# Kernel optimization log

Measured on AMD Instinct MI355X. Metric: run time of the kernel, lower is better.

The kernel has to match this reference:

```python
import jax, jax.numpy as jnp
import numpy as np

T, N = 128, 256
D_T, D_A, D_V = 768, 128, 512
H_T, H_A, H_V = 256, 128, 128
HD = H_T + H_A + H_V      # 512, concat hidden dim
MEM = 256
OUT = 1


def _lstm(x, h, c, Wih, Whh, bih, bhh):
    # torch.nn.LSTMCell: gates = x@Wih^T + bih + h@Whh^T + bhh, chunks (i,f,g,o)
    g = x @ Wih.T + bih + h @ Whh.T + bhh
    i, f, gg, o = jnp.split(g, 4, axis=1)
    c2 = jax.nn.sigmoid(f) * c + jax.nn.sigmoid(i) * jnp.tanh(gg)
    return jax.nn.sigmoid(o) * jnp.tanh(c2), c2


def _mlp(x, w1, b1, w2, b2):
    # Linear -> ReLU -> (dropout: identity in eval) -> Linear
    return jax.nn.relu(x @ w1.T + b1) @ w2.T + b2


def setup_inputs() -> dict:
    key = jax.random.key(0)
    ks = iter(jax.random.split(key, 48))
    def P(shape):
        return jax.random.normal(next(ks), shape, jnp.float32) * 0.05
    inp = {}
    inp["x_text"] = jax.random.normal(next(ks), (T, N, D_T), jnp.float32)
    inp["x_audio"] = jax.random.normal(next(ks), (T, N, D_A), jnp.float32)
    inp["x_vision"] = jax.random.normal(next(ks), (T, N, D_V), jnp.float32)
    inp["lengths"] = jax.random.randint(next(ks), (N,), 1, T + 1, jnp.int32)
    for nm, d, h in (("t", D_T, H_T), ("a", D_A, H_A), ("v", D_V, H_V)):
        inp[f"Wih_{nm}"] = P((4 * h, d))
        inp[f"Whh_{nm}"] = P((4 * h, h))
        inp[f"bih_{nm}"] = P((4 * h,))
        inp[f"bhh_{nm}"] = P((4 * h,))
    # attention MLP: 2*HD -> HD -> 2*HD
    inp["aw1"], inp["ab1"] = P((HD, 2 * HD)), P((HD,))
    inp["aw2"], inp["ab2"] = P((2 * HD, HD)), P((2 * HD,))
    # gamma1 / gamma2 / update MLPs: 2*HD -> HD -> MEM
    for pre in ("g1", "g2", "u"):
        inp[f"{pre}w1"], inp[f"{pre}b1"] = P((HD, 2 * HD)), P((HD,))
        inp[f"{pre}w2"], inp[f"{pre}b2"] = P((MEM, HD)), P((MEM,))
    # output MLP: (HD+MEM) -> (HD+MEM) -> OUT
    inp["ow1"], inp["ob1"] = P((HD + MEM, HD + MEM)), P((HD + MEM,))
    inp["ow2"], inp["ob2"] = P((OUT, HD + MEM)), P((OUT,))
    return inp


def reference(x_text, x_audio, x_vision, lengths,
              Wih_t, Whh_t, bih_t, bhh_t,
              Wih_a, Whh_a, bih_a, bhh_a,
              Wih_v, Whh_v, bih_v, bhh_v,
              aw1, ab1, aw2, ab2,
              g1w1, g1b1, g1w2, g1b2,
              g2w1, g2b1, g2w2, g2b2,
              uw1, ub1, uw2, ub2,
              ow1, ob1, ow2, ob2):
    n = x_text.shape[1]

    def step(carry, xs):
        ht, ct, ha, ca, hv, cv, mem = carry
        xt, xa, xv = xs
        prev_cc = jnp.concatenate([ct, ca, cv], axis=1)           # [N, HD]
        ht, ct = _lstm(xt, ht, ct, Wih_t, Whh_t, bih_t, bhh_t)
        ha, ca = _lstm(xa, ha, ca, Wih_a, Whh_a, bih_a, bhh_a)
        hv, cv = _lstm(xv, hv, cv, Wih_v, Whh_v, bih_v, bhh_v)
        cc = jnp.concatenate([ct, ca, cv], axis=1)                # [N, HD]
        cc_tt = jnp.concatenate([prev_cc, cc], axis=1)            # [N, 2*HD]
        attn = jax.nn.softmax(_mlp(cc_tt, aw1, ab1, aw2, ab2), axis=1)
        cc_star = cc_tt * attn
        g1 = jax.nn.sigmoid(_mlp(cc_star, g1w1, g1b1, g1w2, g1b2))
        g2 = jax.nn.sigmoid(_mlp(cc_star, g2w1, g2b1, g2w2, g2b2))
        u = jnp.tanh(_mlp(cc_star, uw1, ub1, uw2, ub2))
        mem = g1 * mem + g2 * u
        return (ht, ct, ha, ca, hv, cv, mem), (ht, ha, hv, mem)

    z = lambda h: jnp.zeros((n, h), x_text.dtype)
    carry0 = (z(H_T), z(H_T), z(H_A), z(H_A), z(H_V), z(H_V), z(MEM))
    _, (Ht, Ha, Hv, Ms) = jax.lax.scan(step, carry0, (x_text, x_audio, x_vision))

    idx = lengths - 1                 # per-sample last valid step
    rows = jnp.arange(n)
    hT = jnp.concatenate([Ht[idx, rows], Ha[idx, rows], Hv[idx, rows]], axis=1)
    o = jnp.concatenate([hT, Ms[idx, rows]], axis=1)   # [N, HD+MEM]
    return _mlp(o, ow1, ob1, ow2, ob2)
```

## Files before the change

kernel.cpp:

```cpp
#include <hip/hip_runtime.h>
#include <math.h>

#define TT 128
#define NN 256

typedef __attribute__((ext_vector_type(8))) short short8;
typedef __attribute__((ext_vector_type(8))) _Float16 half8;
typedef __attribute__((ext_vector_type(4))) float f32x4;

#define LOG2E 1.44269504088896340736f

__device__ __forceinline__ float exp2_(float x){ return __builtin_amdgcn_exp2f(x); }
__device__ __forceinline__ float rcp_(float x){ return __builtin_amdgcn_rcpf(x); }
__device__ __forceinline__ float sig_(float x){
  return rcp_(1.f + exp2_(-LOG2E*x));
}
__device__ __forceinline__ float tanh_(float x){
  const float e = exp2_(2.f*LOG2E*fabsf(x));
  const float t = 1.f - 2.f*rcp_(e + 1.f);
  return copysignf(t, x);
}
__device__ __forceinline__ float bf2f(unsigned int u){ return __uint_as_float(u<<16); }
__device__ __forceinline__ unsigned short f2bf(float x){
  unsigned int u = __float_as_uint(x);
  u += 0x7fffu + ((u>>16)&1u);
  return (unsigned short)(u>>16);
}
__device__ __forceinline__ unsigned short f2h(float x){
  _Float16 h = (_Float16)x;
  return __builtin_bit_cast(unsigned short, h);
}
__device__ __forceinline__ float h2f(unsigned short u){
  _Float16 h = __builtin_bit_cast(_Float16, u);
  return (float)h;
}
__device__ __forceinline__ unsigned int cvtpk_f16(float a, float b){
  unsigned int r;
  asm("v_cvt_pkrtz_f16_f32 %0, %1, %2" : "=v"(r) : "v"(a), "v"(b));
  return r;
}

__device__ __forceinline__ void gld_lds16(const unsigned short* g, unsigned short* l){
  __builtin_amdgcn_global_load_lds(
      (const __attribute__((address_space(1))) unsigned int*)(g),
      (__attribute__((address_space(3))) unsigned int*)(l), 16, 0, 0);
}

__device__ __forceinline__ short8 ld_llc8s(const unsigned short* p){
  f32x4 r;
  asm volatile("global_load_dwordx4 %0, %1, off sc0 sc1" : "=v"(r) : "v"(p) : "memory");
  return __builtin_bit_cast(short8, r);
}
__device__ __forceinline__ void st_llc_s(unsigned short* p, unsigned short v){
  unsigned int vv = v;
  asm volatile("global_store_short %0, %1, off sc0 sc1" :: "v"(p), "v"(vv) : "memory");
}

template<int BM,int BN,int ACT>
__global__ __launch_bounds__(256) void gemm_nt(const float* __restrict__ A,
    const float* __restrict__ W, const float* __restrict__ b1,
    const float* __restrict__ b2, float* __restrict__ C,
    int M, int K, int Nc)
{
  constexpr int TM = BM/16, TN = BN/16;
  __shared__ float As[BM*32];
  __shared__ float Bs[BN*32];
  const int tid = threadIdx.x;
  const int n0 = blockIdx.x*BN, m0 = blockIdx.y*BM;
  const int tx = tid & 15, ty = tid >> 4;
  float acc[TM][TN];
  #pragma unroll
  for (int r=0;r<TM;r++)
    #pragma unroll
    for (int c=0;c<TN;c++) acc[r][c]=0.f;
  const int swA = (ty & 7) << 2;
  const int swB = (tx & 7) << 2;
  for (int k0=0;k0<K;k0+=32){
    #pragma unroll
    for (int f=tid; f<BM*8; f+=256){
      const int row=f>>3, kq=f&7;
      float4 v = *(const float4*)(A + (size_t)(m0+row)*K + k0 + (kq<<2));
      *(float4*)(&As[row*32 + ((kq<<2) ^ ((row&7)<<2))]) = v;
    }
    #pragma unroll
    for (int f=tid; f<BN*8; f+=256){
      const int row=f>>3, kq=f&7;
      float4 v = *(const float4*)(W + (size_t)(n0+row)*K + k0 + (kq<<2));
      *(float4*)(&Bs[row*32 + ((kq<<2) ^ ((row&7)<<2))]) = v;
    }
    __syncthreads();
    #pragma unroll
    for (int kq=0;kq<8;kq++){
      const int k = kq<<2;
      float4 av[TM], bv[TN];
      #pragma unroll
      for (int r=0;r<TM;r++){ const int row=ty+16*r; av[r] = *(const float4*)(&As[row*32 + (k ^ swA)]); }
      #pragma unroll
      for (int c=0;c<TN;c++){ const int col=tx+16*c; bv[c] = *(const float4*)(&Bs[col*32 + (k ^ swB)]); }
      #pragma unroll
      for (int r=0;r<TM;r++)
        #pragma unroll
        for (int c=0;c<TN;c++){
          acc[r][c] += av[r].x*bv[c].x;
          acc[r][c] += av[r].y*bv[c].y;
          acc[r][c] += av[r].z*bv[c].z;
          acc[r][c] += av[r].w*bv[c].w;
        }
    }
    __syncthreads();
  }
  #pragma unroll
  for (int c=0;c<TN;c++){
    const int gcol = n0 + tx + 16*c;
    const float bias = (b1 ? b1[gcol] : 0.f) + (b2 ? b2[gcol] : 0.f);
    #pragma unroll
    for (int r=0;r<TM;r++){
      const int grow = m0 + ty + 16*r;
      float v = acc[r][c] + bias;
      if (ACT==1) v = fmaxf(v, 0.f);
      C[(size_t)grow*Nc + gcol] = v;
    }
  }
}

template<int ACT,int OBF>
__global__ __launch_bounds__(256) void gemm_mfma(const unsigned short* __restrict__ A,
    const unsigned short* __restrict__ Wb, const float* __restrict__ bias,
    void* __restrict__ Cp, int M, int K, int Nc, int lda, int ldc, int aseg,
    int kswitch, int aextra)
{
  __shared__ unsigned short sA[128*64];
  __shared__ unsigned short sB[128*64];
  const int tid = threadIdx.x;
  const int wave = tid >> 6, lane = tid & 63;
  const int nx = gridDim.x;
  const int lin = blockIdx.y*nx + blockIdx.x;
  const int xcd = lin & 7, s = lin >> 3;
  const int ppx = gridDim.y >> 3;
  const int m0 = (xcd*ppx + s/nx)*128;
  const int n0 = (s % nx)*128;
  const unsigned short* Ab = A + (size_t)(n0 >> 8) * (size_t)aseg;
  const int wm = (wave>>1)*64, wn = (wave&1)*64;
  const int r = lane & 15, g = lane >> 4;
  const int srow = wave*32 + (lane>>3);
  const int scol = (((lane&7) ^ ((lane>>3)&7)) << 3);
  f32x4 acc[4][4];
  #pragma unroll
  for (int i=0;i<4;i++)
    #pragma unroll
    for (int j=0;j<4;j++) acc[i][j] = (f32x4){0.f,0.f,0.f,0.f};

  for (int k0 = 0; k0 < K; k0 += 64){
    const size_t aoff = (size_t)k0 + ((k0 >= kswitch) ? (size_t)aextra : 0);
    #pragma unroll
    for (int i=0;i<4;i++){
      gld_lds16(Ab + (size_t)(m0+srow+i*8)*lda + aoff + scol, &sA[wave*2048 + i*512]);
      gld_lds16(Wb + (size_t)(n0+srow+i*8)*K   + k0   + scol, &sB[wave*2048 + i*512]);
    }
    asm volatile("s_waitcnt vmcnt(0)" ::: "memory");
    __syncthreads();
    #pragma unroll
    for (int ks=0; ks<2; ks++){
      const int cofs = ((ks*32 + g*8) ^ ((r&7)<<3));
      short8 af[4], bfr[4];
      #pragma unroll
      for (int mi=0;mi<4;mi++) af[mi]  = *(const short8*)(&sA[(wm+mi*16+r)*64 + cofs]);
      #pragma unroll
      for (int ni=0;ni<4;ni++) bfr[ni] = *(const short8*)(&sB[(wn+ni*16+r)*64 + cofs]);
      #pragma unroll
      for (int mi=0;mi<4;mi++)
        #pragma unroll
        for (int ni=0;ni<4;ni++)
          acc[mi][ni] = __builtin_amdgcn_mfma_f32_16x16x32_bf16(af[mi], bfr[ni], acc[mi][ni], 0, 0, 0);
    }
    __syncthreads();
  }
  #pragma unroll
  for (int mi=0;mi<4;mi++)
    #pragma unroll
    for (int ni=0;ni<4;ni++){
      const int col_l = wn + ni*16 + r;
      const float b = bias[n0 + col_l];
      #pragma unroll
      for (int reg=0;reg<4;reg++){
        const int row = m0 + wm + mi*16 + g*4 + reg;
        float v = acc[mi][ni][reg] + b;
        if (ACT==1) v = fmaxf(v,0.f);
        else if (ACT==2) v = sig_(v);
        else if (ACT==3) v = tanh_(v);
        else if (ACT==4) v = (n0 + col_l < 512) ? sig_(v) : tanh_(v);
        if (OBF==1)      ((unsigned short*)Cp)[(size_t)row*ldc + n0 + col_l] = f2bf(v);
        else if (OBF==2) ((unsigned short*)Cp)[(size_t)row*ldc + n0 + col_l] = f2h(v);
        else             ((float*)Cp)[(size_t)row*ldc + n0 + col_l] = v;
      }
    }
}

__global__ __launch_bounds__(256) void proj_all(
    const float* __restrict__ xt, const float* __restrict__ xa, const float* __restrict__ xv,
    const unsigned short* __restrict__ wt, const unsigned short* __restrict__ wa,
    const unsigned short* __restrict__ wv,
    const float* __restrict__ bih_t, const float* __restrict__ bhh_t,
    const float* __restrict__ bih_a, const float* __restrict__ bhh_a,
    const float* __restrict__ bih_v, const float* __restrict__ bhh_v,
    unsigned short* __restrict__ Pt, unsigned short* __restrict__ Pa,
    unsigned short* __restrict__ Pv,
    const float* __restrict__ aw1, const float* __restrict__ aw2,
    const float* __restrict__ g1w1, const float* __restrict__ g2w1,
    const float* __restrict__ uw1, const float* __restrict__ g1w2,
    const float* __restrict__ g2w2, const float* __restrict__ uw2,
    unsigned short* __restrict__ wbp)
{
  __shared__ unsigned short sA[128*72];
  __shared__ unsigned short sB[128*64];
  const int tid = threadIdx.x;
  const int blk = blockIdx.x;
  if (blk >= 4096){
    const int cb = blk - 4096;
    const float* src; unsigned short* dst; int i;
    if (cb < 2560){
      const int s = cb >> 9, lb = cb & 511;
      src = (s==0)?aw1:(s==1)?aw2:(s==2)?g1w1:(s==3)?g2w1:uw1;
      dst = wbp + (size_t)s*524288;
      i = lb*256 + tid;
    } else {
      const int s = (cb-2560) >> 7, lb = (cb-2560) & 127;
      src = (s==0)?g1w2:(s==1)?g2w2:uw2;
      dst = wbp + 2621440 + (size_t)s*131072;
      i = lb*256 + tid;
    }
    const float4 v = ((const float4*)src)[i];
    ushort4 o;
    o.x=f2bf(v.x); o.y=f2bf(v.y); o.z=f2bf(v.z); o.w=f2bf(v.w);
    ((ushort4*)dst)[i] = o;
    return;
  }
  const int wave = tid >> 6, lane = tid & 63;
  const float* A; const unsigned short* Wf; const float *b1, *b2; unsigned short* C;
  int K, Nc, nbs, rel, shf;
  if (blk < 2048)      { rel=blk;      A=xt; Wf=wt; b1=bih_t; b2=bhh_t; C=Pt; K=768; Nc=1024; nbs=3; shf=8; }
  else if (blk < 3072) { rel=blk-2048; A=xa; Wf=wa; b1=bih_a; b2=bhh_a; C=Pa; K=128; Nc=512;  nbs=2; shf=7; }
  else                 { rel=blk-3072; A=xv; Wf=wv; b1=bih_v; b2=bhh_v; C=Pv; K=512; Nc=512;  nbs=2; shf=7; }
  const int xcd = rel & 7, s = rel >> 3;
  const int nxc = 1 << nbs;
  const int m0 = (xcd*32 + s/nxc)*128;
  const int n0 = (s & (nxc-1))*128;
  const int wm = (wave>>1)*64, wn = (wave&1)*64;
  const int r = lane & 15, g = lane >> 4;
  const int srow = wave*32 + (lane>>3);
  const int scol = (((lane&7) ^ ((lane>>3)&7)) << 3);
  f32x4 acc[4][4];
  #pragma unroll
  for (int i=0;i<4;i++)
    #pragma unroll
    for (int j=0;j<4;j++) acc[i][j] = (f32x4){0.f,0.f,0.f,0.f};

  for (int k0 = 0; k0 < K; k0 += 64){
    #pragma unroll
    for (int i=0;i<4;i++)
      gld_lds16(Wf + (size_t)(n0+srow+i*8)*K + k0 + scol, &sB[wave*2048 + i*512]);
    #pragma unroll
    for (int j=0;j<4;j++){
      const int slot = tid + j*256;
      const int row = slot>>3, seg = (slot&7)<<3;
      const float* ap = A + (size_t)(m0+row)*K + k0 + seg;
      const float4 v0 = *(const float4*)ap;
      const float4 v1 = *(const float4*)(ap+4);
      uint4 hv;
      hv.x = cvtpk_f16(v0.x, v0.y);
      hv.y = cvtpk_f16(v0.z, v0.w);
      hv.z = cvtpk_f16(v1.x, v1.y);
      hv.w = cvtpk_f16(v1.z, v1.w);
      *(uint4*)(&sA[row*72 + seg]) = hv;
    }
    asm volatile("s_waitcnt vmcnt(0)" ::: "memory");
    __syncthreads();
    #pragma unroll
    for (int ks=0; ks<2; ks++){
      const int cofsB = ((ks*32 + g*8) ^ ((r&7)<<3));
      half8 af[4], bfr[4];
      #pragma unroll
      for (int mi=0;mi<4;mi++) af[mi]  = *(const half8*)(&sA[(wm+mi*16+r)*72 + ks*32 + g*8]);
      #pragma unroll
      for (int ni=0;ni<4;ni++) bfr[ni] = *(const half8*)(&sB[(wn+ni*16+r)*64 + cofsB]);
      #pragma unroll
      for (int mi=0;mi<4;mi++)
        #pragma unroll
        for (int ni=0;ni<4;ni++)
          acc[mi][ni] = __builtin_amdgcn_mfma_f32_16x16x32_f16(af[mi], bfr[ni], acc[mi][ni], 0, 0, 0);
    }
    __syncthreads();
  }
  const int jm = (1<<shf) - 1;
  #pragma unroll
  for (int mi=0;mi<4;mi++)
    #pragma unroll
    for (int ni=0;ni<4;ni++){
      const int col_l = wn + ni*16 + r;
      const int col = n0 + col_l;
      const float b = b1[col] + b2[col];
      const size_t cofs = (size_t)((col & jm)<<2) + (col>>shf);
      #pragma unroll
      for (int reg=0;reg<4;reg++){
        const int row = m0 + wm + mi*16 + g*4 + reg;
        C[(size_t)row*Nc + cofs] = f2h(acc[mi][ni][reg] + b);
      }
    }
}

__device__ __forceinline__ void wfrag_body(const float* __restrict__ W, int H,
    int e, unsigned short* __restrict__ ff)
{
  const int nch = H >> 5;
  const int lane = e & 63;
  int r = e >> 6;
  const int ks = r % nch; r /= nch;
  const int ct = r & 3; r >>= 2;
  const int jb = r;
  const int col = ct*H + jb*16 + (lane & 15);
  const int kb  = ks*32 + (lane >> 4)*8;
  #pragma unroll
  for (int j=0;j<8;j++){
    ff[(size_t)e*8 + j] = f2h(W[(size_t)col*H + kb + j]);
  }
}

__global__ __launch_bounds__(256) void prep_all(
    const float* __restrict__ Wih_t, const float* __restrict__ Wih_a,
    const float* __restrict__ Wih_v,
    const float* __restrict__ Whh_t, const float* __restrict__ Whh_a,
    const float* __restrict__ Whh_v,
    const float* __restrict__ g1b1, const float* __restrict__ g2b1,
    const float* __restrict__ ub1,
    const float* __restrict__ g1b2, const float* __restrict__ g2b2,
    const float* __restrict__ ub2,
    unsigned short* __restrict__ wbp, unsigned short* __restrict__ wfp,
    float* __restrict__ bcat1, float* __restrict__ bcat2,
    float* __restrict__ hfZ,
    unsigned int* __restrict__ flags, unsigned short* __restrict__ ccb)
{
  const int blk = blockIdx.x, tid = threadIdx.x;
  if (blk < 1088){
    const int rel = blk;
    const float* src; unsigned short* dst; int i;
    if (rel < 768)      { src=Wih_t; dst=wbp+3014656; i=rel*256+tid; }
    else if (rel < 832) { src=Wih_a; dst=wbp+3801088; i=(rel-768)*256+tid; }
    else                { src=Wih_v; dst=wbp+3866624; i=(rel-832)*256+tid; }
    const float4 v = ((const float4*)src)[i];
    ushort4 h;
    h.x=f2h(v.x); h.y=f2h(v.y); h.z=f2h(v.z); h.w=f2h(v.w);
    ((ushort4*)dst)[i] = h;
  } else if (blk < 1280){
    const int rel = blk - 1088;
    if (rel < 128)      wfrag_body(Whh_t, 256, rel*256+tid,       wfp);
    else if (rel < 160) wfrag_body(Whh_a, 128, (rel-128)*256+tid, wfp+262144);
    else                wfrag_body(Whh_v, 128, (rel-160)*256+tid, wfp+327680);
  } else {
    const int rel = blk - 1280;
    if (rel < 6){
      const int idx = rel*256 + tid;
      float v = (idx<512) ? g1b1[idx] : (idx<1024) ? g2b1[idx-512] : ub1[idx-1024];
      bcat1[idx] = v;
    } else if (rel < 9){
      const int idx = (rel-6)*256 + tid;
      float v = (idx<256) ? g1b2[idx] : (idx<512) ? g2b2[idx-256] : ub2[idx-512];
      bcat2[idx] = v;
    } else if (rel < 265){
      const int i = (rel-9)*256 + tid;
      ((float4*)hfZ)[i] = (float4){0.f,0.f,0.f,0.f};
    } else if (rel < 271){
      const int i = (rel-265)*256 + tid;
      ((uint4*)flags)[i] = (uint4){0u,0u,0u,0u};
    } else {
      const int i = (rel-271)*256 + tid;
      ((uint4*)ccb)[i] = (uint4){0u,0u,0u,0u};
    }
  }
}

__global__ __launch_bounds__(256) void lstm_scan(
    const unsigned short* __restrict__ Pt, const unsigned short* __restrict__ Pa,
    const unsigned short* __restrict__ Pv,
    const unsigned short* __restrict__ wtfF, const unsigned short* __restrict__ wafF,
    const unsigned short* __restrict__ wvfF,
    const int* __restrict__ lengths,
    unsigned short* __restrict__ hfT, unsigned short* __restrict__ hfA, unsigned short* __restrict__ hfV,
    unsigned short* __restrict__ ccb, float* __restrict__ o_stage,
    unsigned int* __restrict__ flags)
{
  __shared__ unsigned short sWh[16384];
  __shared__ float sG[4*32*17];
  const int tid = threadIdx.x;
  const int b = blockIdx.x;
  const int rb = b & 7, jb = b >> 3;
  const int n0 = rb * 32;
  const unsigned short* P; const unsigned short* wfF; unsigned short* hf;
  int H, j0, off, grp, mem, gsz, jbl;
  if (jb < 16)      { P=Pt; wfF=wtfF; hf=hfT; H=256; jbl=jb;    off=0;   grp=rb;    mem=jbl; gsz=16; }
  else if (jb < 24) { P=Pa; wfF=wafF; hf=hfA; H=128; jbl=jb-16; off=256; grp=8+rb;  mem=jbl; gsz=8;  }
  else              { P=Pv; wfF=wvfF; hf=hfV; H=128; jbl=jb-24; off=384; grp=16+rb; mem=jbl; gsz=8;  }
  j0 = jbl*16;
  const int nch = H >> 5;
  const int G4 = 4*H;
  const size_t planeSz = (size_t)NN*H;
  unsigned int* myflag = &flags[(grp*16+mem)<<4];
  unsigned int* gflags = &flags[(grp*16)<<4];

  {
    const unsigned short* srcF = wfF + (size_t)jbl*4*nch*512;
    const int nseg = 4*nch*64;
    for (int s = tid; s < nseg; s += 256)
      *(uint4*)(&sWh[s*8]) = *(const uint4*)(srcF + (size_t)s*8);
  }
  const int tx = tid & 15, ty = tid >> 4;
  const int n_a = n0 + ty, n_b = n0 + ty + 16;
  const int last_a = lengths[n_a] - 1, last_b = lengths[n_b] - 1;
  const int jcol = j0 + tx;
  const int ksP = jcol >> 5, kqP = (jcol>>3)&3, jP = jcol&7;
  const size_t eA = ((size_t)((rb*2+0)*nch + ksP)*64 + (ty|(kqP<<4)))*8 + jP;
  const size_t eB = ((size_t)((rb*2+1)*nch + ksP)*64 + (ty|(kqP<<4)))*8 + jP;
  const int wave = tid >> 6, lane = tid & 63;
  const int rt = wave >> 1, ct0 = (wave&1)*2, ct1 = ct0+1;
  const size_t fragBase = ((size_t)(rb*2+rt)*nch)*512 + (size_t)lane*8;
  float c_a = 0.f, c_b = 0.f;
  uint2 pA, pB;
  {
    pA = *(const uint2*)(P + (size_t)n_a*G4 + (size_t)jcol*4);
    pB = *(const uint2*)(P + (size_t)n_b*G4 + (size_t)jcol*4);
  }
  __syncthreads();

  for (int t = 0; t < TT; ++t){
    const int cur = t & 1, nxt = cur ^ 1;
    const unsigned short* hH = hf + (size_t)cur*planeSz;
    short8 ah[8];
    #pragma unroll
    for (int ks=0; ks<8; ks++) if (ks < nch)
      ah[ks] = ld_llc8s(hH + fragBase + (size_t)ks*512);
    asm volatile("s_waitcnt vmcnt(0)" ::: "memory");
    uint2 pA2, pB2;
    if (t < TT-1){
      pA2 = *(const uint2*)(P + ((size_t)(t+1)*NN + n_a)*G4 + (size_t)jcol*4);
      pB2 = *(const uint2*)(P + ((size_t)(t+1)*NN + n_b)*G4 + (size_t)jcol*4);
    }
    __builtin_amdgcn_sched_barrier(0);
    f32x4 acc0 = (f32x4){0.f,0.f,0.f,0.f}, acc1 = (f32x4){0.f,0.f,0.f,0.f};
    #pragma unroll
    for (int ks=0; ks<8; ks++) if (ks < nch){
      const int b0 = ((ct0*nch+ks)*64 + lane)*8;
      const int b1 = ((ct1*nch+ks)*64 + lane)*8;
      const half8 w0 = *(const half8*)(&sWh[b0]);
      const half8 w1 = *(const half8*)(&sWh[b1]);
      const half8 a  = __builtin_bit_cast(half8, ah[ks]);
      acc0 = __builtin_amdgcn_mfma_f32_16x16x32_f16(a, w0, acc0, 0,0,0);
      acc1 = __builtin_amdgcn_mfma_f32_16x16x32_f16(a, w1, acc1, 0,0,0);
    }
    #pragma unroll
    for (int reg=0; reg<4; reg++){
      const int grow = rt*16 + (lane>>4)*4 + reg;
      sG[(ct0*32+grow)*17 + (lane&15)] = acc0[reg];
      sG[(ct1*32+grow)*17 + (lane&15)] = acc1[reg];
    }
    __syncthreads();
    const size_t pbase = (size_t)t*NN;
    const int col = off + jcol;
    unsigned short cA, cB; float h2a, h2b;
    {
      unsigned short* dH = hf + (size_t)nxt*planeSz;
      float gi = sG[(0*32+ty)*17+tx] + h2f((unsigned short)(pA.x & 0xffffu));
      float gf = sG[(1*32+ty)*17+tx] + h2f((unsigned short)(pA.x >> 16));
      float gg = sG[(2*32+ty)*17+tx] + h2f((unsigned short)(pA.y & 0xffffu));
      float go = sG[(3*32+ty)*17+tx] + h2f((unsigned short)(pA.y >> 16));
      float c2 = sig_(gf)*c_a + sig_(gi)*tanh_(gg);
      c_a = c2;
      h2a = sig_(go)*tanh_(c2);
      st_llc_s(dH + eA, f2h(h2a));
      cA = f2bf(c2);

      gi = sG[(0*32+ty+16)*17+tx] + h2f((unsigned short)(pB.x & 0xffffu));
      gf = sG[(1*32+ty+16)*17+tx] + h2f((unsigned short)(pB.x >> 16));
      gg = sG[(2*32+ty+16)*17+tx] + h2f((unsigned short)(pB.y & 0xffffu));
      go = sG[(3*32+ty+16)*17+tx] + h2f((unsigned short)(pB.y >> 16));
      c2 = sig_(gf)*c_b + sig_(gi)*tanh_(gg);
      c_b = c2;
      h2b = sig_(go)*tanh_(c2);
      st_llc_s(dH + eB, f2h(h2b));
      cB = f2bf(c2);
    }
    if (t < TT-1){
      const unsigned want = (unsigned)(t+1);
      asm volatile("s_waitcnt vmcnt(0)" ::: "memory");
      __syncthreads();
      if (tid == 0)
        __hip_atomic_store(myflag, want, __ATOMIC_RELAXED, __HIP_MEMORY_SCOPE_SYSTEM);
      ccb[(NN + pbase + n_a)*512 + col] = cA;
      if (t == last_a) o_stage[(size_t)n_a*768 + col] = h2a;
      ccb[(NN + pbase + n_b)*512 + col] = cB;
      if (t == last_b) o_stage[(size_t)n_b*768 + col] = h2b;
      __builtin_amdgcn_sched_barrier(0);
      if (tid < gsz){
        while (__hip_atomic_load(&gflags[tid<<4], __ATOMIC_RELAXED, __HIP_MEMORY_SCOPE_SYSTEM) < want)
          __builtin_amdgcn_s_sleep(1);
      }
      __syncthreads();
      pA = pA2; pB = pB2;
    } else {
      ccb[(NN + pbase + n_a)*512 + col] = cA;
      if (t == last_a) o_stage[(size_t)n_a*768 + col] = h2a;
      ccb[(NN + pbase + n_b)*512 + col] = cB;
      if (t == last_b) o_stage[(size_t)n_b*768 + col] = h2b;
    }
  }
}

__global__ __launch_bounds__(256) void softmax_mul(const unsigned short* __restrict__ logits,
    const unsigned short* __restrict__ ccb, unsigned short* __restrict__ outp)
{
  const int row = blockIdx.x, tid = threadIdx.x;
  const size_t base = (size_t)row*1024 + (tid<<2);
  const ushort4 lv = *(const ushort4*)(logits + base);
  const float v0 = h2f(lv.x), v1 = h2f(lv.y), v2 = h2f(lv.z), v3 = h2f(lv.w);
  float m = fmaxf(fmaxf(v0,v1),fmaxf(v2,v3));
  #pragma unroll
  for (int o=32;o;o>>=1) m = fmaxf(m, __shfl_xor(m, o));
  __shared__ float sm[4]; __shared__ float ss[4];
  const int wid = tid>>6, lane = tid&63;
  if (lane==0) sm[wid]=m;
  __syncthreads();
  m = fmaxf(fmaxf(sm[0],sm[1]),fmaxf(sm[2],sm[3]));
  const float e0 = exp2_((v0-m)*LOG2E), e1 = exp2_((v1-m)*LOG2E);
  const float e2 = exp2_((v2-m)*LOG2E), e3 = exp2_((v3-m)*LOG2E);
  float s = e0+e1+e2+e3;
  #pragma unroll
  for (int o=32;o;o>>=1) s += __shfl_xor(s, o);
  if (lane==0) ss[wid]=s;
  __syncthreads();
  const float inv = rcp_(ss[0]+ss[1]+ss[2]+ss[3]);
  const size_t cbase = (tid < 128)
      ? ((size_t)row*512 + (tid<<2))
      : ((size_t)(row+NN)*512 + (tid<<2) - 512);
  const uint2 c2 = *(const uint2*)(ccb + cbase);
  const float c0 = bf2f(c2.x&0xffffu), c1 = bf2f(c2.x>>16);
  const float c2f= bf2f(c2.y&0xffffu), c3 = bf2f(c2.y>>16);
  uint2 o2;
  o2.x = (unsigned int)f2bf(c0*e0*inv) | ((unsigned int)f2bf(c1*e1*inv)<<16);
  o2.y = (unsigned int)f2bf(c2f*e2*inv) | ((unsigned int)f2bf(c3*e3*inv)<<16);
  *(uint2*)(outp + base) = o2;
}

__global__ __launch_bounds__(256) void mem_scan(const unsigned short* __restrict__ zo,
    const int* __restrict__ lengths, float* __restrict__ o_stage)
{
  const int n = blockIdx.x, j = threadIdx.x;
  const int last = lengths[n]-1;
  float m = 0.f, out = 0.f;
  for (int t0=0;t0<TT;t0+=8){
    unsigned short a[8], bb[8], c[8];
    #pragma unroll
    for (int q=0;q<8;q++){
      const size_t row = ((size_t)(t0+q)*NN + n)*768;
      a[q]  = zo[row+j];
      bb[q] = zo[row+256+j];
      c[q]  = zo[row+512+j];
    }
    #pragma unroll
    for (int q=0;q<8;q++){
      m = h2f(a[q])*m + h2f(bb[q])*h2f(c[q]);
      if (t0+q==last) out = m;
    }
  }
  o_stage[(size_t)n*768 + 512 + j] = out;
}

__global__ __launch_bounds__(256) void out_final(const float* __restrict__ hidden,
    const float* __restrict__ ow2, const float* __restrict__ ob2, float* __restrict__ out)
{
  const int n = blockIdx.x, tid = threadIdx.x;
  const float* hr = hidden + (size_t)n*768;
  float s = hr[tid]*ow2[tid] + hr[tid+256]*ow2[tid+256] + hr[tid+512]*ow2[tid+512];
  #pragma unroll
  for (int o=32;o;o>>=1) s += __shfl_xor(s, o);
  __shared__ float sw[4];
  const int wid=tid>>6, lane=tid&63;
  if (lane==0) sw[wid]=s;
  __syncthreads();
  if (tid==0) out[n] = sw[0]+sw[1]+sw[2]+sw[3] + ob2[0];
}

__global__ void ws_sentinel(float* out, float mb){ out[threadIdx.x] = mb; }

extern "C" void kernel_launch(void* const* d_in, const int* in_sizes, int n_in,
                              void* d_out, int out_size, void* d_ws, size_t ws_size,
                              hipStream_t stream)
{
  const float* x_text   = (const float*)d_in[0];
  const float* x_audio  = (const float*)d_in[1];
  const float* x_vision = (const float*)d_in[2];
  const int*   lengths  = (const int*)d_in[3];
  const float* Wih_t=(const float*)d_in[4],  *Whh_t=(const float*)d_in[5];
  const float* bih_t=(const float*)d_in[6],  *bhh_t=(const float*)d_in[7];
  const float* Wih_a=(const float*)d_in[8],  *Whh_a=(const float*)d_in[9];
  const float* bih_a=(const float*)d_in[10], *bhh_a=(const float*)d_in[11];
  const float* Wih_v=(const float*)d_in[12], *Whh_v=(const float*)d_in[13];
  const float* bih_v=(const float*)d_in[14], *bhh_v=(const float*)d_in[15];
  const float* aw1=(const float*)d_in[16], *ab1=(const float*)d_in[17];
  const float* aw2=(const float*)d_in[18], *ab2=(const float*)d_in[19];
  const float* g1w1=(const float*)d_in[20], *g1b1=(const float*)d_in[21];
  const float* g1w2=(const float*)d_in[22], *g1b2=(const float*)d_in[23];
  const float* g2w1=(const float*)d_in[24], *g2b1=(const float*)d_in[25];
  const float* g2w2=(const float*)d_in[26], *g2b2=(const float*)d_in[27];
  const float* uw1 =(const float*)d_in[28], *ub1 =(const float*)d_in[29];
  const float* uw2 =(const float*)d_in[30], *ub2 =(const float*)d_in[31];
  const float* ow1 =(const float*)d_in[32], *ob1 =(const float*)d_in[33];
  const float* ow2 =(const float*)d_in[34], *ob2 =(const float*)d_in[35];
  (void)in_sizes; (void)n_in; (void)out_size;

  const size_t oPt = 0;
  const size_t oPa = 33554432;
  const size_t oPv = 50331648;
  const size_t oCC = 67108864;
  const size_t oHF = 83886080;
  const size_t oOS = 84148224;
  const size_t oHID= 84344832;
  const size_t oWB = 84541440;
  const size_t oBC = 87162880;
  const size_t oBAR= 87165184;
  const size_t oWF = 87171328;
  const size_t totalf = 87564544;

  if (ws_size < totalf * sizeof(float)) {
    ws_sentinel<<<1,256,0,stream>>>((float*)d_out, (float)(ws_size >> 20));
    return;
  }

  float* ws = (float*)d_ws;
  unsigned short* Pt = (unsigned short*)(ws + oPt);
  unsigned short* Pa = (unsigned short*)(ws + oPa);
  unsigned short* Pv = (unsigned short*)(ws + oPv);
  unsigned short* ccb = (unsigned short*)(ws + oCC);
  unsigned short* hfT = (unsigned short*)(ws + oHF);
  unsigned short* hfA = (unsigned short*)(ws + oHF + 131072);
  unsigned short* hfV = (unsigned short*)(ws + oHF + 196608);
  float* ost = ws + oOS; float* hid = ws + oHID;
  unsigned int* flags = (unsigned int*)(ws + oBAR);
  unsigned short* wbp   = (unsigned short*)(ws + oWB);
  unsigned short* aw1b  = wbp;
  unsigned short* aw2b  = wbp + 524288;
  unsigned short* w1cat = wbp + 1048576;
  unsigned short* w2cat = wbp + 2621440;
  unsigned short* wtih_f= wbp + 3014656;
  unsigned short* waih_f= wbp + 3801088;
  unsigned short* wvih_f= wbp + 3866624;
  float* bcat1 = ws + oBC;
  float* bcat2 = ws + oBC + 1536;
  unsigned short* wfp  = (unsigned short*)(ws + oWF);
  unsigned short* wtfF = wfp;
  unsigned short* wafF = wfp + 262144;
  unsigned short* wvfF = wfp + 327680;
  unsigned short* logits = (unsigned short*)(ws + oPt);
  unsigned short* z1     = (unsigned short*)(ws + oPa);
  unsigned short* ccs    = (unsigned short*)(ws + oPv);
  unsigned short* zcat   = (unsigned short*)(ws + oPt);
  unsigned short* zo     = (unsigned short*)(ws + oPa);

  dim3 blk(256);

  prep_all<<<1615,blk,0,stream>>>(Wih_t, Wih_a, Wih_v, Whh_t, Whh_a, Whh_v,
                                  g1b1, g2b1, ub1, g1b2, g2b2, ub2,
                                  wbp, wfp, bcat1, bcat2, (float*)hfT, flags, ccb);

  proj_all<<<7040,blk,0,stream>>>(x_text, x_audio, x_vision,
                                  wtih_f, waih_f, wvih_f,
                                  bih_t, bhh_t, bih_a, bhh_a, bih_v, bhh_v,
                                  Pt, Pa, Pv,
                                  aw1, aw2, g1w1, g2w1, uw1, g1w2, g2w2, uw2,
                                  wbp);

  {
    void* args[] = {(void*)&Pt,(void*)&Pa,(void*)&Pv,
                    (void*)&wtfF,(void*)&wafF,(void*)&wvfF,
                    (void*)&lengths,(void*)&hfT,(void*)&hfA,(void*)&hfV,
                    (void*)&ccb,(void*)&ost,(void*)&flags};
    hipError_t e = hipLaunchCooperativeKernel((const void*)lstm_scan,
                      dim3(256), dim3(256), args, 0, stream);
    if (e != hipSuccess)
      lstm_scan<<<256,blk,0,stream>>>(Pt,Pa,Pv,wtfF,wafF,wvfF,
                                      lengths,hfT,hfA,hfV,ccb,ost,flags);
  }

  gemm_mfma<1,1><<<dim3(4,256),blk,0,stream>>>(ccb, aw1b, ab1, z1,     32768, 1024, 512,  512, 512, 0, 512, (NN-1)*512);
  gemm_mfma<0,2><<<dim3(8,256),blk,0,stream>>>(z1, aw2b, ab2, logits, 32768, 512,  1024, 512,  1024, 0, 1<<30, 0);
  softmax_mul<<<32768,blk,0,stream>>>(logits, ccb, ccs);
  gemm_mfma<1,1><<<dim3(12,256),blk,0,stream>>>(ccs, w1cat, bcat1, zcat, 32768, 1024, 1536, 1024, 1536, 0, 1<<30, 0);
  gemm_mfma<4,2><<<dim3(6,256),blk,0,stream>>>(zcat, w2cat, bcat2, zo,  32768, 512,  768,  1536, 768, 512, 1<<30, 0);
  mem_scan<<<256,blk,0,stream>>>(zo, lengths, ost);
  gemm_nt<64,64,1><<<dim3(12,4),blk,0,stream>>>(ost, ow1, ob1, nullptr, hid, 256, 768, 768);
  out_final<<<256,blk,0,stream>>>(hid, ow2, ob2, (float*)d_out);
}
```

Before: 902.1 us.

## Compact memory-MLP rows to valid timesteps via row map and skip padded tiles

Adds a build_map kernel that prefix-sums per-sample lengths and builds a row map listing only the (t, n) pairs with t < length. The attention, gate and update GEMMs, softmax, and mem_scan now work over this compacted row set, and blocks past the rounded valid count exit early. Steps after a sample's last valid timestep never affect the output, so this removes roughly half the rows from the post-LSTM GEMM chain when lengths are uniform. It costs one extra single-block launch and gathered A-row loads in the first GEMM.

```diff
diff --git a/kernel.cpp b/kernel.cpp
--- a/kernel.cpp
+++ b/kernel.cpp
@@ -54,6 +54,30 @@
 __device__ __forceinline__ void st_llc_s(unsigned short* p, unsigned short v){
   unsigned int vv = v;
   asm volatile("global_store_short %0, %1, off sc0 sc1" :: "v"(p), "v"(vv) : "memory");
+}
+
+__global__ __launch_bounds__(256) void build_map(const int* __restrict__ lengths,
+    int* __restrict__ base, int* __restrict__ mliv, int* __restrict__ rowmap)
+{
+  const int tid = threadIdx.x;
+  __shared__ int sl[256];
+  __shared__ int sbase[257];
+  sl[tid] = lengths[tid];
+  __syncthreads();
+  if (tid == 0){
+    int acc = 0;
+    for (int n=0;n<256;n++){ sbase[n] = acc; acc += sl[n]; }
+    sbase[256] = acc;
+    mliv[0] = acc;
+    mliv[1] = (acc + 127) & ~127;
+  }
+  __syncthreads();
+  base[tid] = sbase[tid];
+  const int b0 = sbase[tid];
+  const int len = sl[tid];
+  for (int t=0;t<len;t++) rowmap[b0+t] = NN + t*NN + tid;
+  const int M = sbase[256];
+  for (int p = M + tid; p < TT*NN; p += 256) rowmap[p] = NN;
 }
 
 template<int BM,int BN,int ACT>
@@ -123,11 +147,12 @@
   }
 }
 
-template<int ACT,int OBF>
+template<int ACT,int OBF,int AMAP>
 __global__ __launch_bounds__(256) void gemm_mfma(const unsigned short* __restrict__ A,
     const unsigned short* __restrict__ Wb, const float* __restrict__ bias,
     void* __restrict__ Cp, int M, int K, int Nc, int lda, int ldc, int aseg,
-    int kswitch, int aextra)
+    int kswitch, int aextra,
+    const int* __restrict__ rowmap, const int* __restrict__ mliv)
 {
   __shared__ unsigned short sA[128*64];
   __shared__ unsigned short sB[128*64];
@@ -139,11 +164,17 @@
   const int ppx = gridDim.y >> 3;
   const int m0 = (xcd*ppx + s/nx)*128;
   const int n0 = (s % nx)*128;
+  if (m0 >= mliv[1]) return;
   const unsigned short* Ab = A + (size_t)(n0 >> 8) * (size_t)aseg;
   const int wm = (wave>>1)*64, wn = (wave&1)*64;
   const int r = lane & 15, g = lane >> 4;
   const int srow = wave*32 + (lane>>3);
   const int scol = (((lane&7) ^ ((lane>>3)&7)) << 3);
+  int rml[4];
+  if constexpr (AMAP){
+    #pragma unroll
+    for (int i=0;i<4;i++) rml[i] = rowmap[m0 + srow + i*8];
+  }
   f32x4 acc[4][4];
   #pragma unroll
   for (int i=0;i<4;i++)
@@ -151,12 +182,22 @@
     for (int j=0;j<4;j++) acc[i][j] = (f32x4){0.f,0.f,0.f,0.f};
 
   for (int k0 = 0; k0 < K; k0 += 64){
-    const size_t aoff = (size_t)k0 + ((k0 >= kswitch) ? (size_t)aextra : 0);
-    #pragma unroll
-    for (int i=0;i<4;i++){
-      gld_lds16(Ab + (size_t)(m0+srow+i*8)*lda + aoff + scol, &sA[wave*2048 + i*512]);
-      gld_lds16(Wb + (size_t)(n0+srow+i*8)*K   + k0   + scol, &sB[wave*2048 + i*512]);
-    }
+    if constexpr (AMAP){
+      const int sel  = (k0 < kswitch);
+      const int cb   = sel ? k0 : (k0 - kswitch);
+      const int radj = sel ? -NN : 0;
+      #pragma unroll
+      for (int i=0;i<4;i++)
+        gld_lds16(A + (size_t)(rml[i]+radj)*lda + cb + scol, &sA[wave*2048 + i*512]);
+    } else {
+      const size_t aoff = (size_t)k0 + ((k0 >= kswitch) ? (size_t)aextra : 0);
+      #pragma unroll
+      for (int i=0;i<4;i++)
+        gld_lds16(Ab + (size_t)(m0+srow+i*8)*lda + aoff + scol, &sA[wave*2048 + i*512]);
+    }
+    #pragma unroll
+    for (int i=0;i<4;i++)
+      gld_lds16(Wb + (size_t)(n0+srow+i*8)*K + k0 + scol, &sB[wave*2048 + i*512]);
     asm volatile("s_waitcnt vmcnt(0)" ::: "memory");
     __syncthreads();
     #pragma unroll
@@ -514,9 +555,11 @@
 }
 
 __global__ __launch_bounds__(256) void softmax_mul(const unsigned short* __restrict__ logits,
-    const unsigned short* __restrict__ ccb, unsigned short* __restrict__ outp)
+    const unsigned short* __restrict__ ccb, unsigned short* __restrict__ outp,
+    const int* __restrict__ rowmap, const int* __restrict__ mliv)
 {
   const int row = blockIdx.x, tid = threadIdx.x;
+  if (row >= mliv[1]) return;
   const size_t base = (size_t)row*1024 + (tid<<2);
   const ushort4 lv = *(const ushort4*)(logits + base);
   const float v0 = h2f(lv.x), v1 = h2f(lv.y), v2 = h2f(lv.z), v3 = h2f(lv.w);
@@ -536,9 +579,10 @@
   if (lane==0) ss[wid]=s;
   __syncthreads();
   const float inv = rcp_(ss[0]+ss[1]+ss[2]+ss[3]);
+  const int cur = rowmap[row];
   const size_t cbase = (tid < 128)
-      ? ((size_t)row*512 + (tid<<2))
-      : ((size_t)(row+NN)*512 + (tid<<2) - 512);
+      ? ((size_t)(cur - NN)*512 + (tid<<2))
+      : ((size_t)cur*512 + (tid<<2) - 512);
   const uint2 c2 = *(const uint2*)(ccb + cbase);
   const float c0 = bf2f(c2.x&0xffffu), c1 = bf2f(c2.x>>16);
   const float c2f= bf2f(c2.y&0xffffu), c3 = bf2f(c2.y>>16);
@@ -549,27 +593,27 @@
 }
 
 __global__ __launch_bounds__(256) void mem_scan(const unsigned short* __restrict__ zo,
-    const int* __restrict__ lengths, float* __restrict__ o_stage)
+    const int* __restrict__ lengths, const int* __restrict__ base,
+    float* __restrict__ o_stage)
 {
   const int n = blockIdx.x, j = threadIdx.x;
-  const int last = lengths[n]-1;
-  float m = 0.f, out = 0.f;
-  for (int t0=0;t0<TT;t0+=8){
+  const int len = lengths[n];
+  const size_t b0 = (size_t)base[n];
+  float m = 0.f;
+  for (int t0=0; t0<len; t0+=8){
     unsigned short a[8], bb[8], c[8];
     #pragma unroll
     for (int q=0;q<8;q++){
-      const size_t row = ((size_t)(t0+q)*NN + n)*768;
+      const size_t row = (b0 + t0 + q)*768;
       a[q]  = zo[row+j];
       bb[q] = zo[row+256+j];
       c[q]  = zo[row+512+j];
     }
     #pragma unroll
-    for (int q=0;q<8;q++){
-      m = h2f(a[q])*m + h2f(bb[q])*h2f(c[q]);
-      if (t0+q==last) out = m;
-    }
-  }
-  o_stage[(size_t)n*768 + 512 + j] = out;
+    for (int q=0;q<8;q++)
+      if (t0+q < len) m = h2f(a[q])*m + h2f(bb[q])*h2f(c[q]);
+  }
+  o_stage[(size_t)n*768 + 512 + j] = m;
 }
 
 __global__ __launch_bounds__(256) void out_final(const float* __restrict__ hidden,
@@ -626,7 +670,8 @@
   const size_t oBC = 87162880;
   const size_t oBAR= 87165184;
   const size_t oWF = 87171328;
-  const size_t totalf = 87564544;
+  const size_t oMAP= 87564544;
+  const size_t totalf = 87597584;
 
   if (ws_size < totalf * sizeof(float)) {
     ws_sentinel<<<1,256,0,stream>>>((float*)d_out, (float)(ws_size >> 20));
@@ -657,6 +702,9 @@
   unsigned short* wtfF = wfp;
   unsigned short* wafF = wfp + 262144;
   unsigned short* wvfF = wfp + 327680;
+  int* rowmap = (int*)(ws + oMAP);
+  int* basep  = rowmap + 32768;
+  int* mliv   = basep + 256;
   unsigned short* logits = (unsigned short*)(ws + oPt);
   unsigned short* z1     = (unsigned short*)(ws + oPa);
   unsigned short* ccs    = (unsigned short*)(ws + oPv);
@@ -668,6 +716,8 @@
   prep_all<<<1615,blk,0,stream>>>(Wih_t, Wih_a, Wih_v, Whh_t, Whh_a, Whh_v,
                                   g1b1, g2b1, ub1, g1b2, g2b2, ub2,
                                   wbp, wfp, bcat1, bcat2, (float*)hfT, flags, ccb);
+
+  build_map<<<1,blk,0,stream>>>(lengths, basep, mliv, rowmap);
 
   proj_all<<<7040,blk,0,stream>>>(x_text, x_audio, x_vision,
                                   wtih_f, waih_f, wvih_f,
@@ -688,12 +738,12 @@
                                       lengths,hfT,hfA,hfV,ccb,ost,flags);
   }
 
-  gemm_mfma<1,1><<<dim3(4,256),blk,0,stream>>>(ccb, aw1b, ab1, z1,     32768, 1024, 512,  512, 512, 0, 512, (NN-1)*512);
-  gemm_mfma<0,2><<<dim3(8,256),blk,0,stream>>>(z1, aw2b, ab2, logits, 32768, 512,  1024, 512,  1024, 0, 1<<30, 0);
-  softmax_mul<<<32768,blk,0,stream>>>(logits, ccb, ccs);
-  gemm_mfma<1,1><<<dim3(12,256),blk,0,stream>>>(ccs, w1cat, bcat1, zcat, 32768, 1024, 1536, 1024, 1536, 0, 1<<30, 0);
-  gemm_mfma<4,2><<<dim3(6,256),blk,0,stream>>>(zcat, w2cat, bcat2, zo,  32768, 512,  768,  1536, 768, 512, 1<<30, 0);
-  mem_scan<<<256,blk,0,stream>>>(zo, lengths, ost);
+  gemm_mfma<1,1,1><<<dim3(4,256),blk,0,stream>>>(ccb, aw1b, ab1, z1,     32768, 1024, 512,  512, 512, 0, 512, 0, rowmap, mliv);
+  gemm_mfma<0,2,0><<<dim3(8,256),blk,0,stream>>>(z1, aw2b, ab2, logits, 32768, 512,  1024, 512,  1024, 0, 1<<30, 0, rowmap, mliv);
+  softmax_mul<<<32768,blk,0,stream>>>(logits, ccb, ccs, rowmap, mliv);
+  gemm_mfma<1,1,0><<<dim3(12,256),blk,0,stream>>>(ccs, w1cat, bcat1, zcat, 32768, 1024, 1536, 1024, 1536, 0, 1<<30, 0, rowmap, mliv);
+  gemm_mfma<4,2,0><<<dim3(6,256),blk,0,stream>>>(zcat, w2cat, bcat2, zo,  32768, 512,  768,  1536, 768, 512, 1<<30, 0, rowmap, mliv);
+  mem_scan<<<256,blk,0,stream>>>(zo, lengths, basep, ost);
   gemm_nt<64,64,1><<<dim3(12,4),blk,0,stream>>>(ost, ow1, ob1, nullptr, hid, 256, 768, 768);
   out_final<<<256,blk,0,stream>>>(hid, ow2, ob2, (float*)d_out);
 }
```

New measurement: 909.9 us. Within noise of the previous version (+0.9%).
